# Kernel tuning notes

Hardware: AMD Instinct MI355X
Metric: run time of the kernel (lower is better)

## Reference

```python
import jax, jax.numpy as jnp
import numpy as np

N, E, HID, HEADS, KHOPS = 10000, 160000, 64, 8, 3
D = HID // HEADS  # head_dim = 8


def setup_inputs() -> dict:
    key = jax.random.key(0)
    ks = jax.random.split(key, 8)
    s = 1.0 / np.sqrt(HID)
    return {
        "x": jax.random.normal(ks[0], (N, HID), jnp.float32),
        "edge_index": jax.random.randint(ks[1], (2, E), 0, N),
        "edge_feature": jax.random.normal(ks[2], (E, HID), jnp.float32),
        "edge_weight": jax.random.uniform(ks[3], (E,), jnp.float32),
        "Wq": jax.random.normal(ks[4], (HID, HID), jnp.float32) * s,
        "bq": jnp.zeros((HID,), jnp.float32),
        "Wk": jax.random.normal(ks[5], (HID, HID), jnp.float32) * s,
        "bk": jnp.zeros((HID,), jnp.float32),
        "Wv": jax.random.normal(ks[6], (HID, HID), jnp.float32) * s,
        "bv": jnp.zeros((HID,), jnp.float32),
        "hopwise": jnp.ones((KHOPS + 1,), jnp.float32),
    }


def reference(x, edge_index, edge_feature, edge_weight, Wq, bq, Wk, bk, Wv, bv, hopwise):
    n = x.shape[0]
    row, col = edge_index[0], edge_index[1]

    # symmetric degree normalization, scaled by edge_weight
    deg = jax.ops.segment_sum(jnp.ones_like(edge_weight), col, num_segments=n)
    deg_inv = jnp.where(deg > 0, deg ** -0.5, 0.0)
    norm = deg_inv[row] * deg_inv[col] * edge_weight  # [E]

    Q = jax.nn.relu(x @ Wq + bq).reshape(n, HEADS, D)
    K = (x @ Wk + bk).reshape(n, HEADS, D)
    V = (x @ Wv + bv).reshape(n, HEADS, D)
    ef = edge_feature.reshape(-1, HEADS, D)  # [E,h,d]

    hidden = V * hopwise[0]
    sqrt_d = jnp.sqrt(jnp.asarray(D, x.dtype))

    for hop in range(KHOPS):
        if hop == 0:
            Kj = jax.nn.relu(K[row] + ef)                 # [E,h,d]
            # per-edge K (x) V outer product message, scatter-summed at col
            msg = norm[:, None, None, None] * jnp.einsum('ehi,ehj->ehij', Kj, V[row])
            M = jax.ops.segment_sum(msg, col, num_segments=n)   # [N,h,d,d]
            K = jax.ops.segment_sum(norm[:, None, None] * Kj, col, num_segments=n)
        else:
            M = jax.ops.segment_sum(norm[:, None, None, None] * M[row], col, num_segments=n)
            K = jax.ops.segment_sum(norm[:, None, None] * K[row], col, num_segments=n)

        H = jnp.einsum('nhi,nhij->nhj', Q, M)             # [N,h,d]
        nrm = jnp.sqrt(jnp.sum((H / sqrt_d) ** 2, axis=-1))  # [N,h]
        H = H / jnp.maximum(jnp.ones_like(nrm), nrm)[..., None]
        hidden = hidden + hopwise[hop + 1] * H

    return hidden.reshape(n, HEADS * D)
```

## Files before the change

### kernel.cpp

```cpp
#include <hip/hip_runtime.h>
#include <hip/hip_bf16.h>


#define HIDC 64
#define MELEMS 512

__device__ __forceinline__ unsigned bf16rne(float x) {
    unsigned u = __float_as_uint(x);
    return (u + 0x7FFFu + ((u >> 16) & 1u)) >> 16;
}
__device__ __forceinline__ unsigned pack2(float lo, float hi) {
    return bf16rne(lo) | (bf16rne(hi) << 16);
}
__device__ __forceinline__ float bfval(unsigned short v) {
    return __uint_as_float((unsigned)v << 16);
}
__device__ __forceinline__ void acc8(float* acc, float s, uint4 a) {
    acc[0] = fmaf(s, __uint_as_float(a.x << 16), acc[0]);
    acc[1] = fmaf(s, __uint_as_float(a.x & 0xFFFF0000u), acc[1]);
    acc[2] = fmaf(s, __uint_as_float(a.y << 16), acc[2]);
    acc[3] = fmaf(s, __uint_as_float(a.y & 0xFFFF0000u), acc[3]);
    acc[4] = fmaf(s, __uint_as_float(a.z << 16), acc[4]);
    acc[5] = fmaf(s, __uint_as_float(a.z & 0xFFFF0000u), acc[5]);
    acc[6] = fmaf(s, __uint_as_float(a.w << 16), acc[6]);
    acc[7] = fmaf(s, __uint_as_float(a.w & 0xFFFF0000u), acc[7]);
}

__global__ __launch_bounds__(256) void qkv_kernel(
    const float* __restrict__ x,
    const float* __restrict__ Wq, const float* __restrict__ bq,
    const float* __restrict__ Wk, const float* __restrict__ bk,
    const float* __restrict__ Wv, const float* __restrict__ bv,
    const float* __restrict__ hopwise,
    float* __restrict__ Q, float* __restrict__ K,
    unsigned short* __restrict__ Vb,
    float* __restrict__ out, int* __restrict__ deg,
    int* __restrict__ counter, int n) {
    int gid = blockIdx.x * blockDim.x + threadIdx.x;
    if (gid < n) deg[gid] = 0;
    if (gid == 0) *counter = 0;
    int c = gid & 63;
    int nb = (gid >> 6) * 4;
    if (nb >= n) return;
    int mcnt = min(4, n - nb);
    float aq[4], ak[4], av[4];
    #pragma unroll
    for (int m = 0; m < 4; ++m) { aq[m] = bq[c]; ak[m] = bk[c]; av[m] = bv[c]; }
    const float4* x4 = (const float4*)x;
    for (int k4 = 0; k4 < 16; ++k4) {
        float4 xv[4];
        #pragma unroll
        for (int m = 0; m < 4; ++m)
            xv[m] = x4[(size_t)(nb + (m < mcnt ? m : 0)) * 16 + k4];
        #pragma unroll
        for (int kk = 0; kk < 4; ++kk) {
            int k = k4 * 4 + kk;
            float wq = Wq[k * HIDC + c], wk = Wk[k * HIDC + c], wv = Wv[k * HIDC + c];
            #pragma unroll
            for (int m = 0; m < 4; ++m) {
                float xvk = (kk == 0) ? xv[m].x : (kk == 1) ? xv[m].y
                          : (kk == 2) ? xv[m].z : xv[m].w;
                aq[m] = fmaf(xvk, wq, aq[m]);
                ak[m] = fmaf(xvk, wk, ak[m]);
                av[m] = fmaf(xvk, wv, av[m]);
            }
        }
    }
    #pragma unroll
    for (int m = 0; m < 4; ++m) {
        if (m < mcnt) {
            size_t idx = (size_t)(nb + m) * HIDC + c;
            Q[idx] = fmaxf(aq[m], 0.f);
            K[idx] = ak[m];
            Vb[idx] = (unsigned short)bf16rne(av[m]);
            out[idx] = hopwise[0] * av[m];
        }
    }
}

__global__ void deg_kernel(const int* __restrict__ col, int* __restrict__ deg, int e) {
    int i = blockIdx.x * blockDim.x + threadIdx.x;
    if (i < e) atomicAdd(&deg[col[i]], 1);
}

__global__ __launch_bounds__(1024) void base_kernel(const int* __restrict__ deg,
                                                    int* __restrict__ counter,
                                                    int* __restrict__ rowbeg,
                                                    int* __restrict__ cursor, int n) {
    __shared__ int wsum[16];
    __shared__ int blockbase;
    int i = blockIdx.x * 1024 + threadIdx.x;
    int lane = threadIdx.x & 63, w = threadIdx.x >> 6;
    int v = (i < n) ? deg[i] : 0;
    int s = v;
    #pragma unroll
    for (int off = 1; off < 64; off <<= 1) {
        int t = __shfl_up(s, off);
        if (lane >= off) s += t;
    }
    if (lane == 63) wsum[w] = s;
    __syncthreads();
    if (threadIdx.x == 0) {
        int acc = 0;
        #pragma unroll
        for (int w2 = 0; w2 < 16; ++w2) { int t = wsum[w2]; wsum[w2] = acc; acc += t; }
        blockbase = atomicAdd(counter, acc);
    }
    __syncthreads();
    int excl = blockbase + wsum[w] + s - v;
    if (i < n) {
        rowbeg[i] = excl;
        cursor[i] = excl;
    }
}

__global__ __launch_bounds__(256) void stage_kernel(
    const int* __restrict__ row, const int* __restrict__ col,
    const float* __restrict__ ew, const int* __restrict__ deg,
    int* __restrict__ cursor, int* __restrict__ srcrow,
    float* __restrict__ snorm,
    const float* __restrict__ K, const float* __restrict__ ef,
    unsigned short* __restrict__ kjn, int e) {
    int gtid = blockIdx.x * blockDim.x + threadIdx.x;
    int i = gtid >> 4;
    if (i >= e) return;
    int c4 = gtid & 15;
    int lane = threadIdx.x & 63;
    int lb = lane & 48;
    int r = 0, pos = 0;
    float nv = 0.f;
    if (c4 == 0) {
        r = row[i];
        int cc = col[i];
        int dr = deg[r], dc = deg[cc];
        nv = ew[i];
        nv *= (dr > 0) ? rsqrtf((float)dr) : 0.f;
        nv *= (dc > 0) ? rsqrtf((float)dc) : 0.f;
        pos = atomicAdd(&cursor[cc], 1);
        srcrow[pos] = r;
        snorm[pos] = nv;
    }
    r = __shfl(r, lb);
    pos = __shfl(pos, lb);
    nv = __shfl(nv, lb);
    const float4* efv = (const float4*)ef;
    const float4* Kv = (const float4*)K;
    float4 f = efv[(size_t)i * 16 + c4];
    float4 kk = Kv[(size_t)r * 16 + c4];
    uint2 kjp;
    kjp.x = pack2(nv * fmaxf(kk.x + f.x, 0.f), nv * fmaxf(kk.y + f.y, 0.f));
    kjp.y = pack2(nv * fmaxf(kk.z + f.z, 0.f), nv * fmaxf(kk.w + f.w, 0.f));
    ((uint2*)(kjn + (size_t)pos * 64))[c4] = kjp;
}

__device__ __forceinline__ void epilogue64(const float* acc, const float* __restrict__ Q,
                                           float hw, int n, int h, int ii,
                                           float* __restrict__ out) {
    float q = Q[n * HIDC + h * 8 + ii];
    float p[8];
    #pragma unroll
    for (int j = 0; j < 8; ++j) p[j] = q * acc[j];
    #pragma unroll
    for (int off = 1; off < 8; off <<= 1) {
        #pragma unroll
        for (int j = 0; j < 8; ++j) p[j] += __shfl_xor(p[j], off);
    }
    float ssq = 0.f;
    #pragma unroll
    for (int j = 0; j < 8; ++j) ssq = fmaf(p[j], p[j], ssq);
    float nr = sqrtf(ssq * 0.125f);
    float sc = (nr > 1.f) ? (hw / nr) : hw;
    if (ii == 0) {
        float4* o = (float4*)(out + (size_t)n * HIDC + h * 8);
        float4 c0 = o[0], c1 = o[1];
        c0.x = fmaf(p[0], sc, c0.x); c0.y = fmaf(p[1], sc, c0.y);
        c0.z = fmaf(p[2], sc, c0.z); c0.w = fmaf(p[3], sc, c0.w);
        c1.x = fmaf(p[4], sc, c1.x); c1.y = fmaf(p[5], sc, c1.y);
        c1.z = fmaf(p[6], sc, c1.z); c1.w = fmaf(p[7], sc, c1.w);
        o[0] = c0; o[1] = c1;
    }
}

__global__ __launch_bounds__(256) void hop0_kernel(
    const int* __restrict__ rowbeg, const int* __restrict__ deg,
    const int* __restrict__ srcrow, const unsigned short* __restrict__ kjn,
    const unsigned short* __restrict__ Vb,
    const float* __restrict__ Q, const float* __restrict__ hopwise,
    unsigned short* __restrict__ M0, float* __restrict__ out, int nn) {
    int n = blockIdx.x * 4 + (threadIdx.x >> 6);
    if (n >= nn) return;
    int t = threadIdx.x & 63;
    int h = t >> 3, ii = t & 7;
    int beg = rowbeg[n], end = beg + deg[n];
    float acc[8] = {0, 0, 0, 0, 0, 0, 0, 0};
    int k = beg;
    for (; k + 4 <= end; k += 4) {
        int j0 = srcrow[k],     j1 = srcrow[k + 1];
        int j2 = srcrow[k + 2], j3 = srcrow[k + 3];
        float s0 = bfval(kjn[(size_t)(k)     * 64 + t]);
        float s1 = bfval(kjn[(size_t)(k + 1) * 64 + t]);
        float s2 = bfval(kjn[(size_t)(k + 2) * 64 + t]);
        float s3 = bfval(kjn[(size_t)(k + 3) * 64 + t]);
        uint4 v0 = *(const uint4*)(Vb + (size_t)j0 * 64 + h * 8);
        uint4 v1 = *(const uint4*)(Vb + (size_t)j1 * 64 + h * 8);
        uint4 v2 = *(const uint4*)(Vb + (size_t)j2 * 64 + h * 8);
        uint4 v3 = *(const uint4*)(Vb + (size_t)j3 * 64 + h * 8);
        acc8(acc, s0, v0);
        acc8(acc, s1, v1);
        acc8(acc, s2, v2);
        acc8(acc, s3, v3);
    }
    for (; k < end; ++k) {
        float s = bfval(kjn[(size_t)k * 64 + t]);
        uint4 v = *(const uint4*)(Vb + (size_t)srcrow[k] * 64 + h * 8);
        acc8(acc, s, v);
    }
    uint4 st;
    st.x = pack2(acc[0], acc[1]); st.y = pack2(acc[2], acc[3]);
    st.z = pack2(acc[4], acc[5]); st.w = pack2(acc[6], acc[7]);
    ((uint4*)M0)[(size_t)n * 64 + t] = st;
    epilogue64(acc, Q, hopwise[1], n, h, ii, out);
}

__global__ __launch_bounds__(256) void hopk_kernel(
    const int* __restrict__ rowbeg, const int* __restrict__ deg,
    const int* __restrict__ srcrow, const float* __restrict__ snorm,
    const unsigned short* __restrict__ Min, const float* __restrict__ Q,
    const float* __restrict__ hopwise, int hopidx,
    unsigned short* __restrict__ Mout, int writeM, float* __restrict__ out, int nn) {
    int n = blockIdx.x * 4 + (threadIdx.x >> 6);
    if (n >= nn) return;
    int t = threadIdx.x & 63;
    int beg = rowbeg[n], end = beg + deg[n];
    float acc[8] = {0, 0, 0, 0, 0, 0, 0, 0};
    const uint4* Mv = (const uint4*)Min;
    int k = beg;
    for (; k + 8 <= end; k += 8) {
        int j0 = srcrow[k],     j1 = srcrow[k + 1], j2 = srcrow[k + 2], j3 = srcrow[k + 3];
        int j4 = srcrow[k + 4], j5 = srcrow[k + 5], j6 = srcrow[k + 6], j7 = srcrow[k + 7];
        uint4 a0 = Mv[(size_t)j0 * 64 + t];
        uint4 a1 = Mv[(size_t)j1 * 64 + t];
        uint4 a2 = Mv[(size_t)j2 * 64 + t];
        uint4 a3 = Mv[(size_t)j3 * 64 + t];
        uint4 a4 = Mv[(size_t)j4 * 64 + t];
        uint4 a5 = Mv[(size_t)j5 * 64 + t];
        uint4 a6 = Mv[(size_t)j6 * 64 + t];
        uint4 a7 = Mv[(size_t)j7 * 64 + t];
        acc8(acc, snorm[k],     a0);
        acc8(acc, snorm[k + 1], a1);
        acc8(acc, snorm[k + 2], a2);
        acc8(acc, snorm[k + 3], a3);
        acc8(acc, snorm[k + 4], a4);
        acc8(acc, snorm[k + 5], a5);
        acc8(acc, snorm[k + 6], a6);
        acc8(acc, snorm[k + 7], a7);
    }
    for (; k + 4 <= end; k += 4) {
        int j0 = srcrow[k], j1 = srcrow[k + 1], j2 = srcrow[k + 2], j3 = srcrow[k + 3];
        uint4 a0 = Mv[(size_t)j0 * 64 + t];
        uint4 a1 = Mv[(size_t)j1 * 64 + t];
        uint4 a2 = Mv[(size_t)j2 * 64 + t];
        uint4 a3 = Mv[(size_t)j3 * 64 + t];
        acc8(acc, snorm[k],     a0);
        acc8(acc, snorm[k + 1], a1);
        acc8(acc, snorm[k + 2], a2);
        acc8(acc, snorm[k + 3], a3);
    }
    for (; k < end; ++k) acc8(acc, snorm[k], Mv[(size_t)srcrow[k] * 64 + t]);
    if (writeM) {
        uint4 st;
        st.x = pack2(acc[0], acc[1]); st.y = pack2(acc[2], acc[3]);
        st.z = pack2(acc[4], acc[5]); st.w = pack2(acc[6], acc[7]);
        ((uint4*)Mout)[(size_t)n * 64 + t] = st;
    }
    int h = t >> 3, ii = t & 7;
    epilogue64(acc, Q, hopwise[hopidx], n, h, ii, out);
}

extern "C" void kernel_launch(void* const* d_in, const int* in_sizes, int n_in,
                              void* d_out, int out_size, void* d_ws, size_t ws_size,
                              hipStream_t stream) {
    const float* x       = (const float*)d_in[0];
    const int*   ei      = (const int*)d_in[1];
    const float* ef      = (const float*)d_in[2];
    const float* ew      = (const float*)d_in[3];
    const float* Wq      = (const float*)d_in[4];
    const float* bq      = (const float*)d_in[5];
    const float* Wk      = (const float*)d_in[6];
    const float* bk      = (const float*)d_in[7];
    const float* Wv      = (const float*)d_in[8];
    const float* bv      = (const float*)d_in[9];
    const float* hopwise = (const float*)d_in[10];
    float* out = (float*)d_out;

    const int n = in_sizes[0] / HIDC;
    const int e = in_sizes[1] / 2;
    const int* row = ei;
    const int* col = ei + e;

    char* base = (char*)d_ws;
    size_t off = 0;
    auto alloc = [&](size_t bytes) -> void* {
        void* p = base + off;
        off = (off + bytes + 255) & ~(size_t)255;
        return p;
    };
    int*            deg     = (int*)           alloc((size_t)n * 4);
    int*            cursor  = (int*)           alloc((size_t)n * 4);
    int*            rowbeg  = (int*)           alloc((size_t)n * 4);
    int*            counter = (int*)           alloc(256);
    int*            srcrow  = (int*)           alloc((size_t)e * 4);
    float*          snorm   = (float*)         alloc((size_t)e * 4);
    unsigned short* kjn     = (unsigned short*)alloc((size_t)e * HIDC * 2);
    float*          Q       = (float*)         alloc((size_t)n * HIDC * 4);
    float*          K       = (float*)         alloc((size_t)n * HIDC * 4);
    unsigned short* Vb      = (unsigned short*)alloc((size_t)n * HIDC * 2);
    unsigned short* M0      = (unsigned short*)alloc((size_t)n * MELEMS * 2);
    unsigned short* M1      = (unsigned short*)alloc((size_t)n * MELEMS * 2);
    (void)ws_size;

    int qthreads = ((n + 3) / 4) * 64;
    int qb = (qthreads + 255) / 256;
    qkv_kernel<<<qb, 256, 0, stream>>>(x, Wq, bq, Wk, bk, Wv, bv, hopwise,
                                       Q, K, Vb, out, deg, counter, n);

    int eb = (e + 255) / 256;
    deg_kernel<<<eb, 256, 0, stream>>>(col, deg, e);

    int bb = (n + 1023) / 1024;
    base_kernel<<<bb, 1024, 0, stream>>>(deg, counter, rowbeg, cursor, n);

    int sb = ((e * 16) + 255) / 256;
    stage_kernel<<<sb, 256, 0, stream>>>(row, col, ew, deg, cursor,
                                         srcrow, snorm, K, ef, kjn, e);

    int nb = (n + 3) / 4;
    hop0_kernel<<<nb, 256, 0, stream>>>(rowbeg, deg, srcrow, kjn, Vb, Q,
                                        hopwise, M0, out, n);
    hopk_kernel<<<nb, 256, 0, stream>>>(rowbeg, deg, srcrow, snorm, M0, Q, hopwise, 2, M1, 1, out, n);
    hopk_kernel<<<nb, 256, 0, stream>>>(rowbeg, deg, srcrow, snorm, M1, Q, hopwise, 3, M0, 0, out, n);
}
```

Before: 122.4 us.

## Pack edge src/norm into int2, add nontemporal loads, 8 rows per QKV thread

Merges the separate srcrow and snorm arrays into one interleaved int2 edge record, so each CSR edge costs one 8-byte load instead of two 4-byte loads in the hop kernels. Adds nontemporal loads for the single-use edge_feature and kjn streams so they are less likely to evict reused data from cache. Doubles the rows each QKV thread computes from 4 to 8 to reuse the weight loads more. The larger QKV tile raises register use and halves the thread count, and hop0 now reads 8 bytes per edge where it only needs 4.

```diff
diff --git a/kernel.cpp b/kernel.cpp
--- a/kernel.cpp
+++ b/kernel.cpp
@@ -4,6 +4,8 @@
 
 #define HIDC 64
 #define MELEMS 512
+
+typedef float fx4 __attribute__((ext_vector_type(4)));
 
 __device__ __forceinline__ unsigned bf16rne(float x) {
     unsigned u = __float_as_uint(x);
@@ -40,24 +42,24 @@
     if (gid < n) deg[gid] = 0;
     if (gid == 0) *counter = 0;
     int c = gid & 63;
-    int nb = (gid >> 6) * 4;
+    int nb = (gid >> 6) * 8;
     if (nb >= n) return;
-    int mcnt = min(4, n - nb);
-    float aq[4], ak[4], av[4];
-    #pragma unroll
-    for (int m = 0; m < 4; ++m) { aq[m] = bq[c]; ak[m] = bk[c]; av[m] = bv[c]; }
+    int mcnt = min(8, n - nb);
+    float aq[8], ak[8], av[8];
+    #pragma unroll
+    for (int m = 0; m < 8; ++m) { aq[m] = bq[c]; ak[m] = bk[c]; av[m] = bv[c]; }
     const float4* x4 = (const float4*)x;
     for (int k4 = 0; k4 < 16; ++k4) {
-        float4 xv[4];
+        float4 xv[8];
         #pragma unroll
-        for (int m = 0; m < 4; ++m)
+        for (int m = 0; m < 8; ++m)
             xv[m] = x4[(size_t)(nb + (m < mcnt ? m : 0)) * 16 + k4];
         #pragma unroll
         for (int kk = 0; kk < 4; ++kk) {
             int k = k4 * 4 + kk;
             float wq = Wq[k * HIDC + c], wk = Wk[k * HIDC + c], wv = Wv[k * HIDC + c];
             #pragma unroll
-            for (int m = 0; m < 4; ++m) {
+            for (int m = 0; m < 8; ++m) {
                 float xvk = (kk == 0) ? xv[m].x : (kk == 1) ? xv[m].y
                           : (kk == 2) ? xv[m].z : xv[m].w;
                 aq[m] = fmaf(xvk, wq, aq[m]);
@@ -67,7 +69,7 @@
         }
     }
     #pragma unroll
-    for (int m = 0; m < 4; ++m) {
+    for (int m = 0; m < 8; ++m) {
         if (m < mcnt) {
             size_t idx = (size_t)(nb + m) * HIDC + c;
             Q[idx] = fmaxf(aq[m], 0.f);
@@ -117,8 +119,7 @@
 __global__ __launch_bounds__(256) void stage_kernel(
     const int* __restrict__ row, const int* __restrict__ col,
     const float* __restrict__ ew, const int* __restrict__ deg,
-    int* __restrict__ cursor, int* __restrict__ srcrow,
-    float* __restrict__ snorm,
+    int* __restrict__ cursor, int2* __restrict__ erec,
     const float* __restrict__ K, const float* __restrict__ ef,
     unsigned short* __restrict__ kjn, int e) {
     int gtid = blockIdx.x * blockDim.x + threadIdx.x;
@@ -137,15 +138,14 @@
         nv *= (dr > 0) ? rsqrtf((float)dr) : 0.f;
         nv *= (dc > 0) ? rsqrtf((float)dc) : 0.f;
         pos = atomicAdd(&cursor[cc], 1);
-        srcrow[pos] = r;
-        snorm[pos] = nv;
+        erec[pos] = make_int2(r, __float_as_int(nv));
     }
     r = __shfl(r, lb);
     pos = __shfl(pos, lb);
     nv = __shfl(nv, lb);
-    const float4* efv = (const float4*)ef;
+    const fx4* efv = (const fx4*)ef;
     const float4* Kv = (const float4*)K;
-    float4 f = efv[(size_t)i * 16 + c4];
+    fx4 f = __builtin_nontemporal_load(&efv[(size_t)i * 16 + c4]);
     float4 kk = Kv[(size_t)r * 16 + c4];
     uint2 kjp;
     kjp.x = pack2(nv * fmaxf(kk.x + f.x, 0.f), nv * fmaxf(kk.y + f.y, 0.f));
@@ -183,7 +183,7 @@
 
 __global__ __launch_bounds__(256) void hop0_kernel(
     const int* __restrict__ rowbeg, const int* __restrict__ deg,
-    const int* __restrict__ srcrow, const unsigned short* __restrict__ kjn,
+    const int2* __restrict__ erec, const unsigned short* __restrict__ kjn,
     const unsigned short* __restrict__ Vb,
     const float* __restrict__ Q, const float* __restrict__ hopwise,
     unsigned short* __restrict__ M0, float* __restrict__ out, int nn) {
@@ -195,12 +195,12 @@
     float acc[8] = {0, 0, 0, 0, 0, 0, 0, 0};
     int k = beg;
     for (; k + 4 <= end; k += 4) {
-        int j0 = srcrow[k],     j1 = srcrow[k + 1];
-        int j2 = srcrow[k + 2], j3 = srcrow[k + 3];
-        float s0 = bfval(kjn[(size_t)(k)     * 64 + t]);
-        float s1 = bfval(kjn[(size_t)(k + 1) * 64 + t]);
-        float s2 = bfval(kjn[(size_t)(k + 2) * 64 + t]);
-        float s3 = bfval(kjn[(size_t)(k + 3) * 64 + t]);
+        int j0 = erec[k].x,     j1 = erec[k + 1].x;
+        int j2 = erec[k + 2].x, j3 = erec[k + 3].x;
+        float s0 = bfval(__builtin_nontemporal_load(&kjn[(size_t)(k)     * 64 + t]));
+        float s1 = bfval(__builtin_nontemporal_load(&kjn[(size_t)(k + 1) * 64 + t]));
+        float s2 = bfval(__builtin_nontemporal_load(&kjn[(size_t)(k + 2) * 64 + t]));
+        float s3 = bfval(__builtin_nontemporal_load(&kjn[(size_t)(k + 3) * 64 + t]));
         uint4 v0 = *(const uint4*)(Vb + (size_t)j0 * 64 + h * 8);
         uint4 v1 = *(const uint4*)(Vb + (size_t)j1 * 64 + h * 8);
         uint4 v2 = *(const uint4*)(Vb + (size_t)j2 * 64 + h * 8);
@@ -211,8 +211,8 @@
         acc8(acc, s3, v3);
     }
     for (; k < end; ++k) {
-        float s = bfval(kjn[(size_t)k * 64 + t]);
-        uint4 v = *(const uint4*)(Vb + (size_t)srcrow[k] * 64 + h * 8);
+        float s = bfval(__builtin_nontemporal_load(&kjn[(size_t)k * 64 + t]));
+        uint4 v = *(const uint4*)(Vb + (size_t)erec[k].x * 64 + h * 8);
         acc8(acc, s, v);
     }
     uint4 st;
@@ -224,7 +224,7 @@
 
 __global__ __launch_bounds__(256) void hopk_kernel(
     const int* __restrict__ rowbeg, const int* __restrict__ deg,
-    const int* __restrict__ srcrow, const float* __restrict__ snorm,
+    const int2* __restrict__ erec,
     const unsigned short* __restrict__ Min, const float* __restrict__ Q,
     const float* __restrict__ hopwise, int hopidx,
     unsigned short* __restrict__ Mout, int writeM, float* __restrict__ out, int nn) {
@@ -236,37 +236,40 @@
     const uint4* Mv = (const uint4*)Min;
     int k = beg;
     for (; k + 8 <= end; k += 8) {
-        int j0 = srcrow[k],     j1 = srcrow[k + 1], j2 = srcrow[k + 2], j3 = srcrow[k + 3];
-        int j4 = srcrow[k + 4], j5 = srcrow[k + 5], j6 = srcrow[k + 6], j7 = srcrow[k + 7];
-        uint4 a0 = Mv[(size_t)j0 * 64 + t];
-        uint4 a1 = Mv[(size_t)j1 * 64 + t];
-        uint4 a2 = Mv[(size_t)j2 * 64 + t];
-        uint4 a3 = Mv[(size_t)j3 * 64 + t];
-        uint4 a4 = Mv[(size_t)j4 * 64 + t];
-        uint4 a5 = Mv[(size_t)j5 * 64 + t];
-        uint4 a6 = Mv[(size_t)j6 * 64 + t];
-        uint4 a7 = Mv[(size_t)j7 * 64 + t];
-        acc8(acc, snorm[k],     a0);
-        acc8(acc, snorm[k + 1], a1);
-        acc8(acc, snorm[k + 2], a2);
-        acc8(acc, snorm[k + 3], a3);
-        acc8(acc, snorm[k + 4], a4);
-        acc8(acc, snorm[k + 5], a5);
-        acc8(acc, snorm[k + 6], a6);
-        acc8(acc, snorm[k + 7], a7);
+        int2 e0 = erec[k],     e1 = erec[k + 1], e2 = erec[k + 2], e3 = erec[k + 3];
+        int2 e4 = erec[k + 4], e5 = erec[k + 5], e6 = erec[k + 6], e7 = erec[k + 7];
+        uint4 a0 = Mv[(size_t)e0.x * 64 + t];
+        uint4 a1 = Mv[(size_t)e1.x * 64 + t];
+        uint4 a2 = Mv[(size_t)e2.x * 64 + t];
+        uint4 a3 = Mv[(size_t)e3.x * 64 + t];
+        uint4 a4 = Mv[(size_t)e4.x * 64 + t];
+        uint4 a5 = Mv[(size_t)e5.x * 64 + t];
+        uint4 a6 = Mv[(size_t)e6.x * 64 + t];
+        uint4 a7 = Mv[(size_t)e7.x * 64 + t];
+        acc8(acc, __int_as_float(e0.y), a0);
+        acc8(acc, __int_as_float(e1.y), a1);
+        acc8(acc, __int_as_float(e2.y), a2);
+        acc8(acc, __int_as_float(e3.y), a3);
+        acc8(acc, __int_as_float(e4.y), a4);
+        acc8(acc, __int_as_float(e5.y), a5);
+        acc8(acc, __int_as_float(e6.y), a6);
+        acc8(acc, __int_as_float(e7.y), a7);
     }
     for (; k + 4 <= end; k += 4) {
-        int j0 = srcrow[k], j1 = srcrow[k + 1], j2 = srcrow[k + 2], j3 = srcrow[k + 3];
-        uint4 a0 = Mv[(size_t)j0 * 64 + t];
-        uint4 a1 = Mv[(size_t)j1 * 64 + t];
-        uint4 a2 = Mv[(size_t)j2 * 64 + t];
-        uint4 a3 = Mv[(size_t)j3 * 64 + t];
-        acc8(acc, snorm[k],     a0);
-        acc8(acc, snorm[k + 1], a1);
-        acc8(acc, snorm[k + 2], a2);
-        acc8(acc, snorm[k + 3], a3);
-    }
-    for (; k < end; ++k) acc8(acc, snorm[k], Mv[(size_t)srcrow[k] * 64 + t]);
+        int2 e0 = erec[k], e1 = erec[k + 1], e2 = erec[k + 2], e3 = erec[k + 3];
+        uint4 a0 = Mv[(size_t)e0.x * 64 + t];
+        uint4 a1 = Mv[(size_t)e1.x * 64 + t];
+        uint4 a2 = Mv[(size_t)e2.x * 64 + t];
+        uint4 a3 = Mv[(size_t)e3.x * 64 + t];
+        acc8(acc, __int_as_float(e0.y), a0);
+        acc8(acc, __int_as_float(e1.y), a1);
+        acc8(acc, __int_as_float(e2.y), a2);
+        acc8(acc, __int_as_float(e3.y), a3);
+    }
+    for (; k < end; ++k) {
+        int2 e0 = erec[k];
+        acc8(acc, __int_as_float(e0.y), Mv[(size_t)e0.x * 64 + t]);
+    }
     if (writeM) {
         uint4 st;
         st.x = pack2(acc[0], acc[1]); st.y = pack2(acc[2], acc[3]);
@@ -309,8 +312,7 @@
     int*            cursor  = (int*)           alloc((size_t)n * 4);
     int*            rowbeg  = (int*)           alloc((size_t)n * 4);
     int*            counter = (int*)           alloc(256);
-    int*            srcrow  = (int*)           alloc((size_t)e * 4);
-    float*          snorm   = (float*)         alloc((size_t)e * 4);
+    int2*           erec    = (int2*)          alloc((size_t)e * 8);
     unsigned short* kjn     = (unsigned short*)alloc((size_t)e * HIDC * 2);
     float*          Q       = (float*)         alloc((size_t)n * HIDC * 4);
     float*          K       = (float*)         alloc((size_t)n * HIDC * 4);
@@ -319,7 +321,7 @@
     unsigned short* M1      = (unsigned short*)alloc((size_t)n * MELEMS * 2);
     (void)ws_size;
 
-    int qthreads = ((n + 3) / 4) * 64;
+    int qthreads = ((n + 7) / 8) * 64;
     int qb = (qthreads + 255) / 256;
     qkv_kernel<<<qb, 256, 0, stream>>>(x, Wq, bq, Wk, bk, Wv, bv, hopwise,
                                        Q, K, Vb, out, deg, counter, n);
@@ -332,11 +334,11 @@
 
     int sb = ((e * 16) + 255) / 256;
     stage_kernel<<<sb, 256, 0, stream>>>(row, col, ew, deg, cursor,
-                                         srcrow, snorm, K, ef, kjn, e);
+                                         erec, K, ef, kjn, e);
 
     int nb = (n + 3) / 4;
-    hop0_kernel<<<nb, 256, 0, stream>>>(rowbeg, deg, srcrow, kjn, Vb, Q,
+    hop0_kernel<<<nb, 256, 0, stream>>>(rowbeg, deg, erec, kjn, Vb, Q,
                                         hopwise, M0, out, n);
-    hopk_kernel<<<nb, 256, 0, stream>>>(rowbeg, deg, srcrow, snorm, M0, Q, hopwise, 2, M1, 1, out, n);
-    hopk_kernel<<<nb, 256, 0, stream>>>(rowbeg, deg, srcrow, snorm, M1, Q, hopwise, 3, M0, 0, out, n);
-}
+    hopk_kernel<<<nb, 256, 0, stream>>>(rowbeg, deg, erec, M0, Q, hopwise, 2, M1, 1, out, n);
+    hopk_kernel<<<nb, 256, 0, stream>>>(rowbeg, deg, erec, M1, Q, hopwise, 3, M0, 0, out, n);
+}
```

Result: slower. 159.0 us (+29.9%).
